# Optimization experiments

Hardware: AMD Instinct MI355X
Metric: run time of the kernel (lower is better)

The kernel has to match this reference:

```python
import jax, jax.numpy as jnp
import numpy as np

BETA = 0.04
EPS_LOW = 0.2
EPS_HIGH = 0.2
TEMPERATURE = 1.0


def setup_inputs() -> dict:
    key = jax.random.key(0)
    ks = jax.random.split(key, 8)
    B, S, H, V = 4, 1024, 2048, 32000
    return {
        "_input": jax.random.normal(ks[0], (B, S, H), dtype=jnp.float32),
        "lin_weight": jax.random.normal(ks[1], (V, H), dtype=jnp.float32) * 0.02,
        "bias": jax.random.normal(ks[2], (V,), dtype=jnp.float32) * 0.02,
        "selected_token_ids": jax.random.randint(ks[3], (B, S), 0, V),
        "attention_mask": jnp.ones((B, S), dtype=jnp.float32),
        "advantages": jax.random.normal(ks[4], (B,), dtype=jnp.float32),
        "ref_per_token_logps": -jnp.abs(jax.random.normal(ks[5], (B, S), dtype=jnp.float32)),
        "old_per_token_logps": -jnp.abs(jax.random.normal(ks[6], (B, S), dtype=jnp.float32)),
    }


def reference(_input, lin_weight, bias, selected_token_ids, attention_mask,
              advantages, ref_per_token_logps, old_per_token_logps):
    B, S, H = _input.shape
    # fused linear projection to vocab logits: [B,S,V]
    logits = (jnp.einsum("bsh,vh->bsv", _input, lin_weight) + bias) / TEMPERATURE
    log_probs = jax.nn.log_softmax(logits, axis=-1)
    per_token_logps = jnp.take_along_axis(
        log_probs, selected_token_ids[..., None], axis=-1)[..., 0]  # [B,S]

    log_ratio = per_token_logps - old_per_token_logps
    seq_len = jnp.clip(attention_mask.sum(-1), 1.0, None)
    seq_level_log_weight = jax.lax.stop_gradient(
        (log_ratio * attention_mask).sum(-1) / seq_len)[:, None]  # [B,1]

    log_importance_weights = (per_token_logps -
                              jax.lax.stop_gradient(per_token_logps) +
                              seq_level_log_weight)
    coef_1 = jnp.exp(log_importance_weights)
    coef_2 = jnp.clip(coef_1, 1.0 - EPS_LOW, 1.0 + EPS_HIGH)
    adv = advantages[:, None]
    per_token_loss = -jnp.minimum(coef_1 * adv, coef_2 * adv)

    # k3 KL penalty (beta != 0, use_ref_model=True)
    d = ref_per_token_logps - per_token_logps
    kl_div = jnp.exp(d) - d - 1.0
    per_token_loss = per_token_loss + BETA * kl_div

    # loss_type == 'grpo'
    loss = ((per_token_loss * attention_mask).sum(-1) / seq_len).sum() / B
    return loss
```

## Files before the change

### kernel.cpp

```cpp
#include <hip/hip_runtime.h>
#include <hip/hip_bf16.h>

#define BETA_C 0.04f
#define EPS_LOW_C 0.2f
#define EPS_HIGH_C 0.2f

static constexpr int B_ = 4, S_ = 1024, H_ = 2048, V_ = 32000;
static constexpr int M_ = B_ * S_;
static constexpr int BM = 256, BN = 256, BK = 64;
static constexpr int NRB = M_ / BM;
static constexpr int NCB = V_ / BN;
static constexpr int NT  = H_ / BK;

typedef __attribute__((ext_vector_type(8))) short short8;
typedef __attribute__((ext_vector_type(4))) float f32x4;

__device__ __forceinline__ unsigned short f2bf(float f) {
    unsigned u = __builtin_bit_cast(unsigned, f);
    unsigned r = 0x7FFFu + ((u >> 16) & 1u);
    return (unsigned short)((u + r) >> 16);
}

__device__ __forceinline__ void gload_lds16(const unsigned short* g, unsigned short* l) {
    __builtin_amdgcn_global_load_lds(
        (const __attribute__((address_space(1))) unsigned int*)g,
        (__attribute__((address_space(3))) unsigned int*)l, 16, 0, 0);
}

__global__ void cvt_kernel(const float* __restrict__ in, unsigned short* __restrict__ out, int n4) {
    int i = blockIdx.x * blockDim.x + threadIdx.x;
    int stride = gridDim.x * blockDim.x;
    for (; i < n4; i += stride) {
        float4 v = reinterpret_cast<const float4*>(in)[i];
        ushort4 o;
        o.x = f2bf(v.x); o.y = f2bf(v.y); o.z = f2bf(v.z); o.w = f2bf(v.w);
        reinterpret_cast<ushort4*>(out)[i] = o;
    }
}

__global__ __launch_bounds__(512, 2) void gemm_lse_kernel(
    const unsigned short* __restrict__ A,
    const unsigned short* __restrict__ W,
    const float* __restrict__ bias,
    const int* __restrict__ sel,
    float* __restrict__ partials,
    float* __restrict__ sel_logit)
{
    __shared__ __attribute__((aligned(128))) char lds[163840];

    const int bid = blockIdx.x;
    const int swz = (bid & 7) * (NRB * NCB / 8) + (bid >> 3);
    const int brow = swz % NRB;
    const int bcol = swz / NRB;
    const int tid  = threadIdx.x;
    const int lane = tid & 63;
    const int wv   = tid >> 6;
    const int wm   = wv >> 2;
    const int wn   = wv & 3;
    const int l15  = lane & 15, lg = lane >> 4;

    int aOff[8][2];
    #pragma unroll
    for (int m8 = 0; m8 < 8; ++m8)
        #pragma unroll
        for (int ks = 0; ks < 2; ++ks) {
            int row = wm * 128 + m8 * 16 + l15;
            aOff[m8][ks] = row * 128 + (((ks * 4 + lg) ^ (row & 7)) << 4);
        }
    int bOff[4][2];
    #pragma unroll
    for (int n = 0; n < 4; ++n)
        #pragma unroll
        for (int ks = 0; ks < 2; ++ks) {
            int row = wn * 64 + n * 16 + l15;
            bOff[n][ks] = row * 128 + (((ks * 4 + lg) ^ (row & 7)) << 4);
        }

    int sLane[2][2];
    #pragma unroll
    for (int i = 0; i < 2; ++i)
        #pragma unroll
        for (int h = 0; h < 2; ++h) {
            int c = i * 512 + tid;
            int r = (c >> 3) + h * 128;
            int gg = (c & 7) ^ (r & 7);
            sLane[i][h] = r * H_ + gg * 8;
        }

    const unsigned short* Ab = A + (long)brow * BM * H_;
    const unsigned short* Wb = W + (long)bcol * BN * H_;

    f32x4 acc[8][4] = {};
    short8 af[2][2], bfr[4][2];

#define STG(gb, bufoff, h, kt) \
    { _Pragma("unroll") \
      for (int i_ = 0; i_ < 2; ++i_) \
          gload_lds16((gb) + sLane[i_][h] + ((kt) & (H_ - 1)), \
                      (unsigned short*)(lds + (bufoff) + (h) * 16384 + (i_ * 512 + tid) * 16)); }

#define RDA(abase, q) \
    { _Pragma("unroll") \
      for (int mi_ = 0; mi_ < 2; ++mi_) \
      _Pragma("unroll") \
      for (int ks_ = 0; ks_ < 2; ++ks_) \
          af[mi_][ks_] = *(const short8*)(lds + (abase) + aOff[(q) * 2 + mi_][ks_]); }

#define RDB(bbase) \
    { _Pragma("unroll") \
      for (int n_ = 0; n_ < 4; ++n_) \
      _Pragma("unroll") \
      for (int ks_ = 0; ks_ < 2; ++ks_) \
          bfr[n_][ks_] = *(const short8*)(lds + (bbase) + bOff[n_][ks_]); }

#define MM(q) \
    __builtin_amdgcn_s_setprio(1); \
    _Pragma("unroll") \
    for (int ks_ = 0; ks_ < 2; ++ks_) \
    _Pragma("unroll") \
    for (int mi_ = 0; mi_ < 2; ++mi_) \
    _Pragma("unroll") \
    for (int n_ = 0; n_ < 4; ++n_) \
        acc[(q) * 2 + mi_][n_] = __builtin_amdgcn_mfma_f32_16x16x32_bf16( \
            af[mi_][ks_], bfr[n_][ks_], acc[(q) * 2 + mi_][n_], 0, 0, 0); \
    __builtin_amdgcn_s_setprio(0);

#define LGKM(n) asm volatile("s_waitcnt lgkmcnt(" #n ")" ::: "memory");
#define VMC(n)  asm volatile("s_waitcnt vmcnt(" #n ")" ::: "memory");
#define BAR     __builtin_amdgcn_s_barrier();
#define SCB     __builtin_amdgcn_sched_barrier(0);

    STG(Ab, 0, 0, 0)      STG(Ab, 0, 1, 0)
    STG(Wb, 65536, 0, 0)  STG(Wb, 65536, 1, 0)
    STG(Wb, 98304, 0, 64) STG(Wb, 98304, 1, 64)
    VMC(4)
    BAR
    SCB

    int aR = 0,     aW = 32768;
    int bR = 65536, bN = 98304, bW = 131072;
    int ktA = 64, ktB = 128;

    for (int t = 0; t < NT; ++t) {
        RDB(bR) RDA(aR, 0)
        STG(Ab, aW, 0, ktA)
        LGKM(8)
        BAR
        LGKM(0) SCB
        MM(0)
        BAR
        RDA(aR, 1)
        STG(Ab, aW, 1, ktA)
        BAR
        LGKM(0) SCB
        MM(1)
        BAR
        RDA(aR, 2)
        STG(Wb, bW, 0, ktB)
        BAR
        LGKM(0) SCB
        MM(2)
        BAR
        RDA(aR, 3)
        STG(Wb, bW, 1, ktB)
        VMC(4)
        BAR
        LGKM(0) SCB
        MM(3)
        BAR

        int ta = aR; aR = aW; aW = ta;
        int tb = bR; bR = bN; bN = bW; bW = tb;
        ktA += 64; ktB += 64;
    }

    VMC(0)
    __syncthreads();

    float* sums = (float*)lds;
    const int colb = bcol * BN + wn * 64 + l15;
    float bv[4];
    #pragma unroll
    for (int n = 0; n < 4; ++n) bv[n] = bias[colb + n * 16];

    #pragma unroll
    for (int m = 0; m < 8; ++m) {
        #pragma unroll
        for (int j = 0; j < 4; ++j) {
            const long grow = (long)brow * BM + wm * 128 + m * 16 + lg * 4 + j;
            const int stok = sel[grow];
            float s = 0.f;
            #pragma unroll
            for (int n = 0; n < 4; ++n) {
                float logit = acc[m][n][j] + bv[n];
                s += __expf(logit);
                if (stok == colb + n * 16) sel_logit[grow] = logit;
            }
            s += __shfl_xor(s, 1); s += __shfl_xor(s, 2);
            s += __shfl_xor(s, 4); s += __shfl_xor(s, 8);
            if (l15 == 0) sums[(wm * 128 + m * 16 + lg * 4 + j) * 4 + wn] = s;
        }
    }
    __syncthreads();
    if (tid < BM) {
        float tot = sums[tid * 4 + 0] + sums[tid * 4 + 1] + sums[tid * 4 + 2] + sums[tid * 4 + 3];
        partials[((long)brow * BM + tid) * NCB + bcol] = tot;
    }
#undef STG
#undef RDA
#undef RDB
#undef MM
#undef LGKM
#undef VMC
#undef BAR
#undef SCB
}

__global__ void reduce_lse_kernel(const float* __restrict__ partials,
                                  const float* __restrict__ sel_logit,
                                  float* __restrict__ lp) {
    const int row = blockIdx.x;
    const int lane = threadIdx.x;
    float s = 0.f;
    for (int i = lane; i < NCB; i += 64) s += partials[(long)row * NCB + i];
    #pragma unroll
    for (int o = 32; o; o >>= 1) s += __shfl_xor(s, o);
    if (lane == 0) lp[row] = sel_logit[row] - __logf(s);
}

__device__ __forceinline__ float block_sum(float v, float* red) {
    const int lane = threadIdx.x & 63, wid = threadIdx.x >> 6;
    #pragma unroll
    for (int o = 32; o; o >>= 1) v += __shfl_xor(v, o);
    if (lane == 0) red[wid] = v;
    __syncthreads();
    if (wid == 0) {
        float x = (lane < 16) ? red[lane] : 0.f;
        #pragma unroll
        for (int o = 8; o; o >>= 1) x += __shfl_xor(x, o);
        if (lane == 0) red[0] = x;
    }
    __syncthreads();
    float r = red[0];
    __syncthreads();
    return r;
}

__global__ __launch_bounds__(1024) void loss_kernel(
    const float* __restrict__ lp, const float* __restrict__ mask,
    const float* __restrict__ adv, const float* __restrict__ ref,
    const float* __restrict__ old, float* __restrict__ out) {
    __shared__ float red[16];
    const int s = threadIdx.x;
    float loss_acc = 0.f;
    for (int b = 0; b < 4; ++b) {
        const int i = b * S_ + s;
        const float mk = mask[i];
        const float lpv = lp[i];
        const float lrsum = block_sum((lpv - old[i]) * mk, red);
        const float msum  = block_sum(mk, red);
        const float seqlen = fmaxf(msum, 1.f);
        const float sw = lrsum / seqlen;
        const float c1 = __expf(sw);
        const float c2 = fminf(fmaxf(c1, 1.f - EPS_LOW_C), 1.f + EPS_HIGH_C);
        const float a = adv[b];
        const float pmin = fminf(c1 * a, c2 * a);
        const float d = ref[i] - lpv;
        const float ptl = -pmin + BETA_C * (__expf(d) - d - 1.f);
        const float lsum = block_sum(ptl * mk, red);
        loss_acc += lsum / seqlen;
    }
    if (s == 0) out[0] = loss_acc * (1.f / (float)B_);
}

extern "C" void kernel_launch(void* const* d_in, const int* in_sizes, int n_in,
                              void* d_out, int out_size, void* d_ws, size_t ws_size,
                              hipStream_t stream) {
    const float* x    = (const float*)d_in[0];
    const float* W    = (const float*)d_in[1];
    const float* bias = (const float*)d_in[2];
    const int*   sel  = (const int*)d_in[3];
    const float* mask = (const float*)d_in[4];
    const float* adv  = (const float*)d_in[5];
    const float* ref  = (const float*)d_in[6];
    const float* old  = (const float*)d_in[7];
    float* out = (float*)d_out;

    char* ws = (char*)d_ws;
    unsigned short* Abf = (unsigned short*)ws;
    unsigned short* Wbf = (unsigned short*)(ws + 16777216);
    float* partials  = (float*)(ws + 16777216 + 131072000);
    float* sel_logit = (float*)(ws + 16777216 + 131072000 + 2048000);
    float* lp        = sel_logit + M_;

    cvt_kernel<<<2048, 256, 0, stream>>>(x, Abf, M_ * H_ / 4);
    cvt_kernel<<<4096, 256, 0, stream>>>(W, Wbf, V_ * H_ / 4);

    gemm_lse_kernel<<<NRB * NCB, 512, 0, stream>>>(Abf, Wbf, bias, sel, partials, sel_logit);

    reduce_lse_kernel<<<M_, 64, 0, stream>>>(partials, sel_logit, lp);
    loss_kernel<<<1, 1024, 0, stream>>>(lp, mask, adv, ref, old, out);
}
```

Before: 568.8 us.

## Switch GEMM inner loop to 32x32x16 bf16 MFMA tiles

Replaces the 16x16x32 MFMA instructions with 32x32x16 MFMA. Each wave now holds 4x2 accumulator tiles of 16 floats instead of 8x4 tiles of 4 floats, and the LDS fragment offsets are recomputed for the new operand layout. B fragments are now re-read per k-quarter together with A. The aim is fewer LDS reads per FLOP and fewer MFMA issues. The epilogue is remapped to the 32x32 output layout and adds an extra shuffle stage to the row reduction.

```diff
diff --git a/kernel.cpp b/kernel.cpp
--- a/kernel.cpp
+++ b/kernel.cpp
@@ -13,7 +13,7 @@
 static constexpr int NT  = H_ / BK;
 
 typedef __attribute__((ext_vector_type(8))) short short8;
-typedef __attribute__((ext_vector_type(4))) float f32x4;
+typedef __attribute__((ext_vector_type(16))) float f32x16;
 
 __device__ __forceinline__ unsigned short f2bf(float f) {
     unsigned u = __builtin_bit_cast(unsigned, f);
@@ -57,23 +57,23 @@
     const int wv   = tid >> 6;
     const int wm   = wv >> 2;
     const int wn   = wv & 3;
-    const int l15  = lane & 15, lg = lane >> 4;
-
-    int aOff[8][2];
-    #pragma unroll
-    for (int m8 = 0; m8 < 8; ++m8)
-        #pragma unroll
-        for (int ks = 0; ks < 2; ++ks) {
-            int row = wm * 128 + m8 * 16 + l15;
-            aOff[m8][ks] = row * 128 + (((ks * 4 + lg) ^ (row & 7)) << 4);
-        }
-    int bOff[4][2];
-    #pragma unroll
-    for (int n = 0; n < 4; ++n)
-        #pragma unroll
-        for (int ks = 0; ks < 2; ++ks) {
-            int row = wn * 64 + n * 16 + l15;
-            bOff[n][ks] = row * 128 + (((ks * 4 + lg) ^ (row & 7)) << 4);
+    const int l31  = lane & 31, hi = lane >> 5;
+
+    int aOff[4][4];
+    #pragma unroll
+    for (int mt = 0; mt < 4; ++mt)
+        #pragma unroll
+        for (int q = 0; q < 4; ++q) {
+            int row = wm * 128 + mt * 32 + l31;
+            aOff[mt][q] = row * 128 + (((2 * q + hi) ^ (row & 7)) << 4);
+        }
+    int bOff[2][4];
+    #pragma unroll
+    for (int nt = 0; nt < 2; ++nt)
+        #pragma unroll
+        for (int q = 0; q < 4; ++q) {
+            int row = wn * 64 + nt * 32 + l31;
+            bOff[nt][q] = row * 128 + (((2 * q + hi) ^ (row & 7)) << 4);
         }
 
     int sLane[2][2];
@@ -90,8 +90,8 @@
     const unsigned short* Ab = A + (long)brow * BM * H_;
     const unsigned short* Wb = W + (long)bcol * BN * H_;
 
-    f32x4 acc[8][4] = {};
-    short8 af[2][2], bfr[4][2];
+    f32x16 acc[4][2] = {};
+    short8 af[4], bf[2];
 
 #define STG(gb, bufoff, h, kt) \
     { _Pragma("unroll") \
@@ -101,31 +101,26 @@
 
 #define RDA(abase, q) \
     { _Pragma("unroll") \
-      for (int mi_ = 0; mi_ < 2; ++mi_) \
-      _Pragma("unroll") \
-      for (int ks_ = 0; ks_ < 2; ++ks_) \
-          af[mi_][ks_] = *(const short8*)(lds + (abase) + aOff[(q) * 2 + mi_][ks_]); }
-
-#define RDB(bbase) \
+      for (int mt_ = 0; mt_ < 4; ++mt_) \
+          af[mt_] = *(const short8*)(lds + (abase) + aOff[mt_][q]); }
+
+#define RDB(bbase, q) \
     { _Pragma("unroll") \
-      for (int n_ = 0; n_ < 4; ++n_) \
-      _Pragma("unroll") \
-      for (int ks_ = 0; ks_ < 2; ++ks_) \
-          bfr[n_][ks_] = *(const short8*)(lds + (bbase) + bOff[n_][ks_]); }
-
-#define MM(q) \
+      for (int nt_ = 0; nt_ < 2; ++nt_) \
+          bf[nt_] = *(const short8*)(lds + (bbase) + bOff[nt_][q]); }
+
+#define MM() \
     __builtin_amdgcn_s_setprio(1); \
     _Pragma("unroll") \
-    for (int ks_ = 0; ks_ < 2; ++ks_) \
+    for (int mt_ = 0; mt_ < 4; ++mt_) \
     _Pragma("unroll") \
-    for (int mi_ = 0; mi_ < 2; ++mi_) \
-    _Pragma("unroll") \
-    for (int n_ = 0; n_ < 4; ++n_) \
-        acc[(q) * 2 + mi_][n_] = __builtin_amdgcn_mfma_f32_16x16x32_bf16( \
-            af[mi_][ks_], bfr[n_][ks_], acc[(q) * 2 + mi_][n_], 0, 0, 0); \
+    for (int nt_ = 0; nt_ < 2; ++nt_) \
+        acc[mt_][nt_] = __builtin_amdgcn_mfma_f32_32x32x16_bf16( \
+            af[mt_], bf[nt_], acc[mt_][nt_], 0, 0, 0); \
     __builtin_amdgcn_s_setprio(0);
 
-#define LGKM(n) asm volatile("s_waitcnt lgkmcnt(" #n ")" ::: "memory");
+#define LGKM0   asm volatile("s_waitcnt lgkmcnt(0)" ::: "memory"); \
+    __builtin_amdgcn_sched_barrier(0);
 #define VMC(n)  asm volatile("s_waitcnt vmcnt(" #n ")" ::: "memory");
 #define BAR     __builtin_amdgcn_s_barrier();
 #define SCB     __builtin_amdgcn_sched_barrier(0);
@@ -142,31 +137,30 @@
     int ktA = 64, ktB = 128;
 
     for (int t = 0; t < NT; ++t) {
-        RDB(bR) RDA(aR, 0)
+        RDA(aR, 0) RDB(bR, 0)
         STG(Ab, aW, 0, ktA)
-        LGKM(8)
-        BAR
-        LGKM(0) SCB
-        MM(0)
-        BAR
-        RDA(aR, 1)
+        BAR
+        LGKM0
+        MM()
+        BAR
+        RDA(aR, 1) RDB(bR, 1)
         STG(Ab, aW, 1, ktA)
         BAR
-        LGKM(0) SCB
-        MM(1)
-        BAR
-        RDA(aR, 2)
+        LGKM0
+        MM()
+        BAR
+        RDA(aR, 2) RDB(bR, 2)
         STG(Wb, bW, 0, ktB)
         BAR
-        LGKM(0) SCB
-        MM(2)
-        BAR
-        RDA(aR, 3)
+        LGKM0
+        MM()
+        BAR
+        RDA(aR, 3) RDB(bR, 3)
         STG(Wb, bW, 1, ktB)
         VMC(4)
         BAR
-        LGKM(0) SCB
-        MM(3)
+        LGKM0
+        MM()
         BAR
 
         int ta = aR; aR = aW; aW = ta;
@@ -178,27 +172,27 @@
     __syncthreads();
 
     float* sums = (float*)lds;
-    const int colb = bcol * BN + wn * 64 + l15;
-    float bv[4];
-    #pragma unroll
-    for (int n = 0; n < 4; ++n) bv[n] = bias[colb + n * 16];
-
-    #pragma unroll
-    for (int m = 0; m < 8; ++m) {
-        #pragma unroll
-        for (int j = 0; j < 4; ++j) {
-            const long grow = (long)brow * BM + wm * 128 + m * 16 + lg * 4 + j;
+    const int colb = bcol * BN + wn * 64 + l31;
+    float bv[2] = { bias[colb], bias[colb + 32] };
+
+    #pragma unroll
+    for (int mt = 0; mt < 4; ++mt) {
+        #pragma unroll
+        for (int reg = 0; reg < 16; ++reg) {
+            const int rl = wm * 128 + mt * 32 + (reg & 3) + 8 * (reg >> 2) + 4 * hi;
+            const long grow = (long)brow * BM + rl;
             const int stok = sel[grow];
             float s = 0.f;
             #pragma unroll
-            for (int n = 0; n < 4; ++n) {
-                float logit = acc[m][n][j] + bv[n];
+            for (int nt = 0; nt < 2; ++nt) {
+                float logit = acc[mt][nt][reg] + bv[nt];
                 s += __expf(logit);
-                if (stok == colb + n * 16) sel_logit[grow] = logit;
+                if (stok == colb + nt * 32) sel_logit[grow] = logit;
             }
             s += __shfl_xor(s, 1); s += __shfl_xor(s, 2);
             s += __shfl_xor(s, 4); s += __shfl_xor(s, 8);
-            if (l15 == 0) sums[(wm * 128 + m * 16 + lg * 4 + j) * 4 + wn] = s;
+            s += __shfl_xor(s, 16);
+            if (l31 == 0) sums[rl * 4 + wn] = s;
         }
     }
     __syncthreads();
@@ -210,7 +204,7 @@
 #undef RDA
 #undef RDB
 #undef MM
-#undef LGKM
+#undef LGKM0
 #undef VMC
 #undef BAR
 #undef SCB
```

Measured after the change: 686.6 us. +20.7%, slower.
